# Optimization experiments

Hardware: AMD Instinct MI355X
Metric: run time of the kernel (lower is better)

The kernel has to match this reference:

```python
import jax, jax.numpy as jnp
import numpy as np

OUT_DIM = 65536
G = 2            # num_global_crops
L = 8            # num_local_crops
T = G + L        # num_total_crops
B = 64           # batch_size
STUDENT_TEMP = 0.1
TEACHER_TEMP = 0.04
CENTER_MOMENTUM = 0.9


def setup_inputs() -> dict:
    key = jax.random.key(0)
    k1, k2 = jax.random.split(key)
    student_output = jax.random.normal(k1, (B * T, OUT_DIM), dtype=jnp.float32)
    teacher_output = jax.random.normal(k2, (B * G, OUT_DIM), dtype=jnp.float32)
    center = jnp.zeros((1, OUT_DIM), dtype=jnp.float32)
    return {
        "student_output": student_output,
        "teacher_output": teacher_output,
        "center": center,
        "batch_size": B,
        "epoch": 0,
    }


def reference(student_output, teacher_output, center, batch_size, epoch):
    # Teacher temperature schedule: epoch < warmup_epochs(=0) never true -> teacher_temp
    teacher_temp = TEACHER_TEMP

    # (B, T, D) scaled student logits
    s = (student_output / STUDENT_TEMP).reshape(batch_size, T, -1)
    # (B, G, D) teacher softmax probabilities
    t_probs = jax.nn.softmax(teacher_output / teacher_temp, axis=-1).reshape(batch_size, G, -1)

    # Center update (buffer is updated BEFORE being used, matching the torch code)
    batch_center = jnp.mean(t_probs.reshape(-1, t_probs.shape[-1]), axis=0, keepdims=True)  # (1, D)
    new_center = center * CENTER_MOMENTUM + batch_center * (1.0 - CENTER_MOMENTUM)
    t_centered = t_probs - new_center  # broadcast (1,D) over (B,G,D)

    # Stable log-softmax over student crops: (B, T, D)
    logp = jax.nn.log_softmax(s, axis=-1)

    # Cross terms for all (teacher crop g, student crop t) pairs, summed over batch:
    # cross[b, g, t] = -sum_d t_centered[b,g,d] * logp[b,t,d]
    cross = -jnp.einsum("bgd,btd->bgt", t_centered, logp)  # (B, G, T)

    # Skip same-view pairs (s_idx == t_idx and s_idx < G), i.e. diagonal of the GxG block
    mask = jnp.ones((G, T), dtype=cross.dtype).at[jnp.arange(G), jnp.arange(G)].set(0.0)
    total_loss = jnp.sum(cross * mask)

    n_loss_terms = batch_size * G * (T - 1)
    return jnp.reshape(total_loss / n_loss_terms, (1,))
```

## Files before the change

### kernel.cpp

```cpp
#include <hip/hip_runtime.h>
#include <math.h>

#define SE_OFF  16
#define DOT_OFF 704
#define SP_OFF  1024
#define NC_OFF  2048

constexpr float INV_ST = 10.0f;
constexpr float INV_TT = 25.0f;
constexpr float CS = 64.0f;
constexpr float CT = 100.0f;

typedef float v4f __attribute__((ext_vector_type(4)));

__device__ __forceinline__ float wave_sum(float v) {
#pragma unroll
    for (int off = 32; off > 0; off >>= 1) v += __shfl_down(v, off, 64);
    return v;
}

__global__ void __launch_bounds__(256) k1_rowsum(
        const float* __restrict__ te, float* __restrict__ ws) {
    int bid = blockIdx.x;
    int tid = threadIdx.x;
    if (bid < 384 && tid < 2) ws[bid * 2 + tid] = 0.0f;
    int r = bid >> 2, ch = bid & 3;
    const float4* p = (const float4*)te + (size_t)r * 16384 + ch * 4096;
    float se = 0.0f;
#pragma unroll 4
    for (int i = 0; i < 16; ++i) {
        float4 v = p[tid + (i << 8)];
        se += __expf(fmaf(v.x, INV_TT, -CT));
        se += __expf(fmaf(v.y, INV_TT, -CT));
        se += __expf(fmaf(v.z, INV_TT, -CT));
        se += __expf(fmaf(v.w, INV_TT, -CT));
    }
    se = wave_sum(se);
    __shared__ float ls[4];
    int lane = tid & 63, wv = tid >> 6;
    if (lane == 0) ls[wv] = se;
    __syncthreads();
    if (tid == 0) ws[SP_OFF + bid] = ls[0] + ls[1] + ls[2] + ls[3];
}

__global__ void __launch_bounds__(256) k2_nc(
        const float* __restrict__ te, const float* __restrict__ center,
        float* __restrict__ ws) {
    __shared__ float rS[128];
    int tid = threadIdx.x;
    if (tid < 128) {
        float s = ws[SP_OFF + tid * 4] + ws[SP_OFF + tid * 4 + 1]
                + ws[SP_OFF + tid * 4 + 2] + ws[SP_OFF + tid * 4 + 3];
        rS[tid] = 1.0f / s;
    }
    __syncthreads();
    int d = blockIdx.x * 256 + tid;
    float a = 0.0f;
#pragma unroll 8
    for (int r = 0; r < 128; ++r) {
        float u = te[((size_t)r << 16) + d];
        a += __expf(fmaf(u, INV_TT, -CT)) * rS[r];
    }
    float ncv = fmaf(0.9f, center[d], a * (1.0f / 1280.0f));
    ws[NC_OFF + d] = ncv;
    float s = wave_sum(ncv);
    __shared__ float ls[4];
    int lane = tid & 63, wv = tid >> 6;
    if (lane == 0) ls[wv] = s;
    __syncthreads();
    if (tid == 0) atomicAdd(&ws[0], ls[0] + ls[1] + ls[2] + ls[3]);
}

__global__ void __launch_bounds__(256, 4) k3_fused(
        const float* __restrict__ st, const float* __restrict__ te,
        float* __restrict__ ws) {
    int bid = blockIdx.x;
    int b = bid >> 5, ch = bid & 31;
    int ra = 2 * b, rb = ra + 1;
    float Sa = ws[SP_OFF + ra * 4] + ws[SP_OFF + ra * 4 + 1]
             + ws[SP_OFF + ra * 4 + 2] + ws[SP_OFF + ra * 4 + 3];
    float Sb = ws[SP_OFF + rb * 4] + ws[SP_OFF + rb * 4 + 1]
             + ws[SP_OFF + rb * 4 + 2] + ws[SP_OFF + rb * 4 + 3];
    float rsa = 1.0f / Sa, rsb = 1.0f / Sb;

    int tid = threadIdx.x;
    size_t fbase = (size_t)ch * 512 + tid;
    const float4* ta = (const float4*)te + (size_t)ra * 16384 + fbase;
    const float4* tb = (const float4*)te + (size_t)rb * 16384 + fbase;
    const float4* nc = (const float4*)(ws + NC_OFF) + fbase;

    float4 c0[2], c1[2], cL[2];
#pragma unroll
    for (int k = 0; k < 2; ++k) {
        float4 av = ta[k * 256], bv = tb[k * 256], nv = nc[k * 256];
        float pa, pb;
        pa = __expf(fmaf(av.x, INV_TT, -CT)) * rsa;
        pb = __expf(fmaf(bv.x, INV_TT, -CT)) * rsb;
        c0[k].x = (nv.x - pb) * INV_ST; c1[k].x = (nv.x - pa) * INV_ST;
        cL[k].x = c0[k].x + c1[k].x;
        pa = __expf(fmaf(av.y, INV_TT, -CT)) * rsa;
        pb = __expf(fmaf(bv.y, INV_TT, -CT)) * rsb;
        c0[k].y = (nv.y - pb) * INV_ST; c1[k].y = (nv.y - pa) * INV_ST;
        cL[k].y = c0[k].y + c1[k].y;
        pa = __expf(fmaf(av.z, INV_TT, -CT)) * rsa;
        pb = __expf(fmaf(bv.z, INV_TT, -CT)) * rsb;
        c0[k].z = (nv.z - pb) * INV_ST; c1[k].z = (nv.z - pa) * INV_ST;
        cL[k].z = c0[k].z + c1[k].z;
        pa = __expf(fmaf(av.w, INV_TT, -CT)) * rsa;
        pb = __expf(fmaf(bv.w, INV_TT, -CT)) * rsb;
        c0[k].w = (nv.w - pb) * INV_ST; c1[k].w = (nv.w - pa) * INV_ST;
        cL[k].w = c0[k].w + c1[k].w;
    }

    const v4f* xbase = (const v4f*)st + (size_t)(b * 10) * 16384 + fbase;
    float q = 0.0f;
    float se[10];
#pragma unroll
    for (int t = 0; t < 10; ++t) se[t] = 0.0f;

    auto do_row = [&](int t, const float4 (&cf)[2], float& acc) {
        const v4f* xr = xbase + (size_t)t * 16384;
#pragma unroll
        for (int k = 0; k < 2; ++k) {
            v4f xv = __builtin_nontemporal_load(xr + k * 256);
            q = fmaf(cf[k].x, xv.x, q); acc += __expf(fmaf(xv.x, INV_ST, -CS));
            q = fmaf(cf[k].y, xv.y, q); acc += __expf(fmaf(xv.y, INV_ST, -CS));
            q = fmaf(cf[k].z, xv.z, q); acc += __expf(fmaf(xv.z, INV_ST, -CS));
            q = fmaf(cf[k].w, xv.w, q); acc += __expf(fmaf(xv.w, INV_ST, -CS));
        }
    };

    do_row(0, c0, se[0]);
    do_row(1, c1, se[1]);
#pragma unroll
    for (int t = 2; t < 10; ++t) do_row(t, cL, se[t]);

#pragma unroll
    for (int t = 0; t < 10; ++t) se[t] = wave_sum(se[t]);
    q = wave_sum(q);
    __shared__ float red[4][11];
    int lane = tid & 63, wv = tid >> 6;
    if (lane == 0) {
#pragma unroll
        for (int t = 0; t < 10; ++t) red[wv][t] = se[t];
        red[wv][10] = q;
    }
    __syncthreads();
    if (tid < 11) {
        float v = red[0][tid] + red[1][tid] + red[2][tid] + red[3][tid];
        if (tid < 10) atomicAdd(&ws[SE_OFF + b * 10 + tid], v);
        else          atomicAdd(&ws[DOT_OFF + b], v);
    }
}

__global__ void __launch_bounds__(640) k4_final(
        const float* __restrict__ ws, float* __restrict__ out) {
    int tid = threadIdx.x;
    int t = tid % 10;
    float w = (t < 2) ? 1.0f : 2.0f;
    float zv = w * (CS + __logf(ws[SE_OFF + tid]));
    float dv = (tid < 64) ? ws[DOT_OFF + tid] : 0.0f;
    zv = wave_sum(zv);
    dv = wave_sum(dv);
    __shared__ float lz[10], ldt[10];
    int lane = tid & 63, wv = tid >> 6;
    if (lane == 0) { lz[wv] = zv; ldt[wv] = dv; }
    __syncthreads();
    if (tid == 0) {
        float zs = 0.0f, ds = 0.0f;
#pragma unroll
        for (int i = 0; i < 10; ++i) { zs += lz[i]; ds += ldt[i]; }
        out[0] = (ds + (1.0f - ws[0]) * zs) * (1.0f / 1152.0f);
    }
}

extern "C" void kernel_launch(void* const* d_in, const int* in_sizes, int n_in,
                              void* d_out, int out_size, void* d_ws, size_t ws_size,
                              hipStream_t stream) {
    const float* st = (const float*)d_in[0];
    const float* te = (const float*)d_in[1];
    const float* center = (const float*)d_in[2];
    float* ws = (float*)d_ws;
    float* out = (float*)d_out;

    hipLaunchKernelGGL(k1_rowsum, dim3(512), dim3(256), 0, stream, te, ws);
    hipLaunchKernelGGL(k2_nc, dim3(256), dim3(256), 0, stream, te, center, ws);
    hipLaunchKernelGGL(k3_fused, dim3(2048), dim3(256), 0, stream, st, te, ws);
    hipLaunchKernelGGL(k4_final, dim3(1), dim3(640), 0, stream, ws, out);
}
```

Before: 265.2 us.

## Split center accumulation across row groups with atomics and halve per-block work in main kernel

The center-accumulation kernel now splits rows into 8 groups per column chunk, uses float4 loads, and combines partial sums with atomicAdds into a buffer pre-initialized by the first kernel. The center-sum reduction moves into the main fused kernel, which now launches twice as many blocks, each handling one float4 per row. The aim is more parallelism and better coalescing in the center pass, at the cost of extra atomics and fewer loads in flight per thread in the main kernel.

```diff
diff --git a/kernel.cpp b/kernel.cpp
--- a/kernel.cpp
+++ b/kernel.cpp
@@ -20,14 +20,16 @@
 }
 
 __global__ void __launch_bounds__(256) k1_rowsum(
-        const float* __restrict__ te, float* __restrict__ ws) {
+        const float* __restrict__ te, const float* __restrict__ center,
+        float* __restrict__ ws) {
     int bid = blockIdx.x;
     int tid = threadIdx.x;
     if (bid < 384 && tid < 2) ws[bid * 2 + tid] = 0.0f;
+    if (tid < 128) ws[NC_OFF + bid * 128 + tid] = 0.9f * center[bid * 128 + tid];
     int r = bid >> 2, ch = bid & 3;
     const float4* p = (const float4*)te + (size_t)r * 16384 + ch * 4096;
     float se = 0.0f;
-#pragma unroll 4
+#pragma unroll
     for (int i = 0; i < 16; ++i) {
         float4 v = p[tid + (i << 8)];
         se += __expf(fmaf(v.x, INV_TT, -CT));
@@ -44,38 +46,44 @@
 }
 
 __global__ void __launch_bounds__(256) k2_nc(
-        const float* __restrict__ te, const float* __restrict__ center,
-        float* __restrict__ ws) {
-    __shared__ float rS[128];
+        const float* __restrict__ te, float* __restrict__ ws) {
+    __shared__ float rS[16];
     int tid = threadIdx.x;
-    if (tid < 128) {
-        float s = ws[SP_OFF + tid * 4] + ws[SP_OFF + tid * 4 + 1]
-                + ws[SP_OFF + tid * 4 + 2] + ws[SP_OFF + tid * 4 + 3];
+    int bid = blockIdx.x;
+    int dch = bid >> 3, rq = bid & 7;
+    int r0 = rq * 16;
+    if (tid < 16) {
+        int r = r0 + tid;
+        float s = ws[SP_OFF + r * 4] + ws[SP_OFF + r * 4 + 1]
+                + ws[SP_OFF + r * 4 + 2] + ws[SP_OFF + r * 4 + 3];
         rS[tid] = 1.0f / s;
     }
     __syncthreads();
-    int d = blockIdx.x * 256 + tid;
-    float a = 0.0f;
-#pragma unroll 8
-    for (int r = 0; r < 128; ++r) {
-        float u = te[((size_t)r << 16) + d];
-        a += __expf(fmaf(u, INV_TT, -CT)) * rS[r];
+    size_t d4 = (size_t)dch * 256 + tid;
+    const float4* te4 = (const float4*)te;
+    float ax = 0.0f, ay = 0.0f, az = 0.0f, aw = 0.0f;
+#pragma unroll
+    for (int i = 0; i < 16; ++i) {
+        float4 v = te4[(size_t)(r0 + i) * 16384 + d4];
+        float w = rS[i];
+        ax += __expf(fmaf(v.x, INV_TT, -CT)) * w;
+        ay += __expf(fmaf(v.y, INV_TT, -CT)) * w;
+        az += __expf(fmaf(v.z, INV_TT, -CT)) * w;
+        aw += __expf(fmaf(v.w, INV_TT, -CT)) * w;
     }
-    float ncv = fmaf(0.9f, center[d], a * (1.0f / 1280.0f));
-    ws[NC_OFF + d] = ncv;
-    float s = wave_sum(ncv);
-    __shared__ float ls[4];
-    int lane = tid & 63, wv = tid >> 6;
-    if (lane == 0) ls[wv] = s;
-    __syncthreads();
-    if (tid == 0) atomicAdd(&ws[0], ls[0] + ls[1] + ls[2] + ls[3]);
+    constexpr float SC = 1.0f / 1280.0f;
+    float* ncp = ws + NC_OFF + d4 * 4;
+    atomicAdd(ncp + 0, ax * SC);
+    atomicAdd(ncp + 1, ay * SC);
+    atomicAdd(ncp + 2, az * SC);
+    atomicAdd(ncp + 3, aw * SC);
 }
 
 __global__ void __launch_bounds__(256, 4) k3_fused(
         const float* __restrict__ st, const float* __restrict__ te,
         float* __restrict__ ws) {
     int bid = blockIdx.x;
-    int b = bid >> 5, ch = bid & 31;
+    int b = bid >> 6, ch = bid & 63;
     int ra = 2 * b, rb = ra + 1;
     float Sa = ws[SP_OFF + ra * 4] + ws[SP_OFF + ra * 4 + 1]
              + ws[SP_OFF + ra * 4 + 2] + ws[SP_OFF + ra * 4 + 3];
@@ -84,32 +92,31 @@
     float rsa = 1.0f / Sa, rsb = 1.0f / Sb;
 
     int tid = threadIdx.x;
-    size_t fbase = (size_t)ch * 512 + tid;
-    const float4* ta = (const float4*)te + (size_t)ra * 16384 + fbase;
-    const float4* tb = (const float4*)te + (size_t)rb * 16384 + fbase;
-    const float4* nc = (const float4*)(ws + NC_OFF) + fbase;
+    size_t fbase = (size_t)ch * 256 + tid;
+    float4 av = ((const float4*)te)[(size_t)ra * 16384 + fbase];
+    float4 bv = ((const float4*)te)[(size_t)rb * 16384 + fbase];
+    float4 nv = ((const float4*)(ws + NC_OFF))[fbase];
 
-    float4 c0[2], c1[2], cL[2];
-#pragma unroll
-    for (int k = 0; k < 2; ++k) {
-        float4 av = ta[k * 256], bv = tb[k * 256], nv = nc[k * 256];
+    if (b == 0) {
+        float cs = wave_sum(nv.x + nv.y + nv.z + nv.w);
+        if ((tid & 63) == 0) atomicAdd(&ws[0], cs);
+    }
+
+    float4 c0, c1, cL;
+    {
         float pa, pb;
         pa = __expf(fmaf(av.x, INV_TT, -CT)) * rsa;
         pb = __expf(fmaf(bv.x, INV_TT, -CT)) * rsb;
-        c0[k].x = (nv.x - pb) * INV_ST; c1[k].x = (nv.x - pa) * INV_ST;
-        cL[k].x = c0[k].x + c1[k].x;
+        c0.x = (nv.x - pb) * INV_ST; c1.x = (nv.x - pa) * INV_ST; cL.x = c0.x + c1.x;
         pa = __expf(fmaf(av.y, INV_TT, -CT)) * rsa;
         pb = __expf(fmaf(bv.y, INV_TT, -CT)) * rsb;
-        c0[k].y = (nv.y - pb) * INV_ST; c1[k].y = (nv.y - pa) * INV_ST;
-        cL[k].y = c0[k].y + c1[k].y;
+        c0.y = (nv.y - pb) * INV_ST; c1.y = (nv.y - pa) * INV_ST; cL.y = c0.y + c1.y;
         pa = __expf(fmaf(av.z, INV_TT, -CT)) * rsa;
         pb = __expf(fmaf(bv.z, INV_TT, -CT)) * rsb;
-        c0[k].z = (nv.z - pb) * INV_ST; c1[k].z = (nv.z - pa) * INV_ST;
-        cL[k].z = c0[k].z + c1[k].z;
+        c0.z = (nv.z - pb) * INV_ST; c1.z = (nv.z - pa) * INV_ST; cL.z = c0.z + c1.z;
         pa = __expf(fmaf(av.w, INV_TT, -CT)) * rsa;
         pb = __expf(fmaf(bv.w, INV_TT, -CT)) * rsb;
-        c0[k].w = (nv.w - pb) * INV_ST; c1[k].w = (nv.w - pa) * INV_ST;
-        cL[k].w = c0[k].w + c1[k].w;
+        c0.w = (nv.w - pb) * INV_ST; c1.w = (nv.w - pa) * INV_ST; cL.w = c0.w + c1.w;
     }
 
     const v4f* xbase = (const v4f*)st + (size_t)(b * 10) * 16384 + fbase;
@@ -118,16 +125,12 @@
 #pragma unroll
     for (int t = 0; t < 10; ++t) se[t] = 0.0f;
 
-    auto do_row = [&](int t, const float4 (&cf)[2], float& acc) {
-        const v4f* xr = xbase + (size_t)t * 16384;
-#pragma unroll
-        for (int k = 0; k < 2; ++k) {
-            v4f xv = __builtin_nontemporal_load(xr + k * 256);
-            q = fmaf(cf[k].x, xv.x, q); acc += __expf(fmaf(xv.x, INV_ST, -CS));
-            q = fmaf(cf[k].y, xv.y, q); acc += __expf(fmaf(xv.y, INV_ST, -CS));
-            q = fmaf(cf[k].z, xv.z, q); acc += __expf(fmaf(xv.z, INV_ST, -CS));
-            q = fmaf(cf[k].w, xv.w, q); acc += __expf(fmaf(xv.w, INV_ST, -CS));
-        }
+    auto do_row = [&](int t, const float4& cf, float& acc) {
+        v4f xv = __builtin_nontemporal_load(xbase + (size_t)t * 16384);
+        q = fmaf(cf.x, xv.x, q); acc += __expf(fmaf(xv.x, INV_ST, -CS));
+        q = fmaf(cf.y, xv.y, q); acc += __expf(fmaf(xv.y, INV_ST, -CS));
+        q = fmaf(cf.z, xv.z, q); acc += __expf(fmaf(xv.z, INV_ST, -CS));
+        q = fmaf(cf.w, xv.w, q); acc += __expf(fmaf(xv.w, INV_ST, -CS));
     };
 
     do_row(0, c0, se[0]);
@@ -183,8 +186,8 @@
     float* ws = (float*)d_ws;
     float* out = (float*)d_out;
 
-    hipLaunchKernelGGL(k1_rowsum, dim3(512), dim3(256), 0, stream, te, ws);
-    hipLaunchKernelGGL(k2_nc, dim3(256), dim3(256), 0, stream, te, center, ws);
-    hipLaunchKernelGGL(k3_fused, dim3(2048), dim3(256), 0, stream, st, te, ws);
+    hipLaunchKernelGGL(k1_rowsum, dim3(512), dim3(256), 0, stream, te, center, ws);
+    hipLaunchKernelGGL(k2_nc, dim3(512), dim3(256), 0, stream, te, ws);
+    hipLaunchKernelGGL(k3_fused, dim3(4096), dim3(256), 0, stream, st, te, ws);
     hipLaunchKernelGGL(k4_final, dim3(1), dim3(640), 0, stream, ws, out);
 }
```

Measured after the change: 275.5 us. 1.04x slower.
